# Optimization experiments

Measured on AMD Instinct MI355X. Metric: run time of the kernel, lower is better.

The kernel has to match this reference:

```python
import jax, jax.numpy as jnp
import numpy as np

N = 100000   # nodes
E = 1600000  # edges
IN = 41      # in_channels (21 atom + 20 residue)
ED = 8       # edge_dim
H = 64       # hidden_dim
L = 3        # num_layers
G = 256      # graphs in batch
ATOM = 21
EPS = 1e-5   # GraphNorm eps


def setup_inputs() -> dict:
    key = jax.random.key(0)
    ks = jax.random.split(key, 32)
    s = 0.1
    x = jax.random.normal(ks[0], (N, IN), jnp.float32)
    # make even-index nodes 'ligand' atoms (zero residue part) so both MLP branches fire
    lig = (jnp.arange(N) % 2) == 0
    x = x.at[:, ATOM:].set(jnp.where(lig[:, None], 0.0, x[:, ATOM:]))
    edge_index = jax.random.randint(ks[1], (2, E), 0, N)
    edge_attr = jax.random.normal(ks[2], (E, ED), jnp.float32)
    batch = jnp.sort(jax.random.randint(ks[3], (N,), 0, G))
    p = {
        "lig_W1": s * jax.random.normal(ks[4], (IN, H), jnp.float32),
        "lig_b1": jnp.zeros((H,), jnp.float32),
        "lig_W2": s * jax.random.normal(ks[5], (H, H), jnp.float32),
        "lig_b2": jnp.zeros((H,), jnp.float32),
        "prot_W1": s * jax.random.normal(ks[6], (IN, H), jnp.float32),
        "prot_b1": jnp.zeros((H,), jnp.float32),
        "prot_W2": s * jax.random.normal(ks[7], (H, H), jnp.float32),
        "prot_b2": jnp.zeros((H,), jnp.float32),
        # per-layer stacked params for the 3 GINEConv + GraphNorm blocks
        "conv_We": s * jax.random.normal(ks[8], (L, ED, H), jnp.float32),
        "conv_be": jnp.zeros((L, H), jnp.float32),
        "conv_W1": s * jax.random.normal(ks[9], (L, H, H), jnp.float32),
        "conv_b1": jnp.zeros((L, H), jnp.float32),
        "conv_W2": s * jax.random.normal(ks[10], (L, H, H), jnp.float32),
        "conv_b2": jnp.zeros((L, H), jnp.float32),
        "norm_w": jnp.ones((L, H), jnp.float32),
        "norm_b": jnp.zeros((L, H), jnp.float32),
        "norm_a": jnp.ones((L, H), jnp.float32),  # mean_scale alpha
        "out_W1": s * jax.random.normal(ks[11], (H, H), jnp.float32),
        "out_b1": jnp.zeros((H,), jnp.float32),
        "out_W2": s * jax.random.normal(ks[12], (H, 1), jnp.float32),
        "out_b2": jnp.zeros((1,), jnp.float32),
    }
    return dict(x=x, edge_index=edge_index, edge_attr=edge_attr, batch=batch, **p)


def reference(x, edge_index, edge_attr, batch,
              lig_W1, lig_b1, lig_W2, lig_b2,
              prot_W1, prot_b1, prot_W2, prot_b2,
              conv_We, conv_be, conv_W1, conv_b1, conv_W2, conv_b2,
              norm_w, norm_b, norm_a,
              out_W1, out_b1, out_W2, out_b2):
    # --- input encoder: ligand vs protein branch by residue-part mask ---
    res_mask = jnp.sum(jnp.abs(x[:, ATOM:]), axis=1) > 1e-6
    h_lig = jax.nn.relu(jax.nn.relu(x @ lig_W1 + lig_b1) @ lig_W2 + lig_b2)
    h_prot = jax.nn.relu(jax.nn.relu(x @ prot_W1 + prot_b1) @ prot_W2 + prot_b2)
    h = jnp.where(res_mask[:, None], h_prot, h_lig)  # [N, H]

    src, dst = edge_index[0], edge_index[1]
    counts = jnp.maximum(jax.ops.segment_sum(jnp.ones((N,), h.dtype), batch,
                                             num_segments=G), 1.0)[:, None]  # [G,1]

    for l in range(L):
        # GINEConv (eps=0): nn(h_i + sum_j relu(h_j + lin(e_ij)))
        e = edge_attr @ conv_We[l] + conv_be[l]           # [E, H]
        msg = jax.nn.relu(h[src] + e)                     # [E, H]
        aggr = jax.ops.segment_sum(msg, dst, num_segments=N)
        z = h + aggr
        h = jax.nn.relu(z @ conv_W1[l] + conv_b1[l]) @ conv_W2[l] + conv_b2[l]
        # GraphNorm: (h - alpha*mean_g) / sqrt(var_g + eps) * w + b
        mean = jax.ops.segment_sum(h, batch, num_segments=G) / counts  # [G, H]
        out = h - norm_a[l] * mean[batch]
        var = jax.ops.segment_sum(out * out, batch, num_segments=G) / counts
        h = norm_w[l] * (out / jnp.sqrt(var + EPS)[batch]) + norm_b[l]
        h = jax.nn.relu(h)

    # global_add_pool + readout (dropout = identity at eval)
    g = jax.ops.segment_sum(h, batch, num_segments=G)  # [G, H]
    out = jax.nn.relu(g @ out_W1 + out_b1) @ out_W2 + out_b2  # [G, 1]
    return out.reshape(-1)
```

## Files before the change

### kernel.cpp

```cpp
#include <hip/hip_runtime.h>

#define NN 100000
#define NE 1600000
#define IN_CH 41
#define EDIM 8
#define H 64
#define GNUM 256
#define ATOM 21
#define EPSV 1e-5f
#define EPW 16
#define NTILE (NN / 16)

#define BSH 9
#define NBK 196
#define DPB 512
#define VPT 8
#define EPB (256 * VPT)
#define NBLK_E ((NE + EPB - 1) / EPB)
#define EPB_P1 (1024 * VPT)
#define NBLK_P1 ((NE + EPB_P1 - 1) / EPB_P1)

typedef unsigned short u16;
typedef unsigned int u32;
typedef unsigned long long u64;
typedef __attribute__((ext_vector_type(8))) short short8;
typedef __attribute__((ext_vector_type(4))) float floatx4;

__device__ __forceinline__ u16 f2bf(float f) {
    u32 u = __float_as_uint(f);
    u32 r = (u + 0x7FFFu + ((u >> 16) & 1u)) >> 16;
    return (u16)r;
}
__device__ __forceinline__ float bf2f(u16 u) {
    return __uint_as_float(((u32)u) << 16);
}
__device__ __forceinline__ floatx4 mfma16(short8 a, short8 b, floatx4 c) {
    return __builtin_amdgcn_mfma_f32_16x16x32_bf16(a, b, c, 0, 0, 0);
}
__device__ __forceinline__ short8 pack_bf8(float4 a, float4 b) {
    short8 s;
    s[0] = (short)f2bf(a.x); s[1] = (short)f2bf(a.y);
    s[2] = (short)f2bf(a.z); s[3] = (short)f2bf(a.w);
    s[4] = (short)f2bf(b.x); s[5] = (short)f2bf(b.y);
    s[6] = (short)f2bf(b.z); s[7] = (short)f2bf(b.w);
    return s;
}

__global__ __launch_bounds__(256) void partition_kernel(
    const float* __restrict__ x, int* __restrict__ ctr,
    int* __restrict__ lig_list, int* __restrict__ prot_list)
{
    const int n = blockIdx.x * 256 + threadIdx.x;
    const int lane = threadIdx.x & 63;
    float m = 0.0f;
    if (n < NN) {
        const float* xr = x + (size_t)n * IN_CH + ATOM;
#pragma unroll
        for (int d = 0; d < IN_CH - ATOM; ++d) m += fabsf(xr[d]);
    }
    const bool valid = n < NN;
    const bool prot = valid && (m > 1e-6f);
    const bool lig = valid && !prot;

    const u64 bl = __ballot(lig);
    const u64 bp = __ballot(prot);
    const u64 below_m = (lane == 63) ? (~0ull >> 1) : ((1ull << lane) - 1ull);
    int base_l = 0, base_p = 0;
    if (lane == 0) {
        if (bl) base_l = atomicAdd(&ctr[0], (int)__popcll(bl));
        if (bp) base_p = atomicAdd(&ctr[1], (int)__popcll(bp));
    }
    base_l = __shfl(base_l, 0, 64);
    base_p = __shfl(base_p, 0, 64);
    if (lig)  lig_list [base_l + (int)__popcll(bl & below_m)] = n;
    if (prot) prot_list[base_p + (int)__popcll(bp & below_m)] = n;
}

__global__ __launch_bounds__(256) void xb_kernel(
    const float* __restrict__ x, u16* __restrict__ xb)
{
    const int id = blockIdx.x * 256 + threadIdx.x;
    if (id >= NN * H) return;
    const int n = id >> 6, d = id & 63;
    xb[id] = (d < IN_CH) ? f2bf(x[(size_t)n * IN_CH + d]) : (u16)0;
}

__global__ __launch_bounds__(256) void prep_w_kernel(
    const float* __restrict__ ligW1, const float* __restrict__ ligW2,
    const float* __restrict__ protW1, const float* __restrict__ protW2,
    const float* __restrict__ convW1, const float* __restrict__ convW2,
    u16* __restrict__ wf)
{
    const int id = blockIdx.x * 256 + threadIdx.x;
    if (id >= 10 * 4096) return;
    const int j = id & 7, l = (id >> 3) & 63, t = (id >> 9) & 3;
    const int c = (id >> 11) & 1, mat = id >> 12;
    const int k = c * 32 + ((l >> 4) * 8) + j;
    const int n = t * 16 + (l & 15);
    const float* src; int K = 64;
    if (mat == 0)      { src = ligW1;  K = IN_CH; }
    else if (mat == 1) { src = ligW2; }
    else if (mat == 2) { src = protW1; K = IN_CH; }
    else if (mat == 3) { src = protW2; }
    else {
        const int layer = (mat - 4) >> 1;
        src = (((mat - 4) & 1) ? convW2 : convW1) + (size_t)layer * H * H;
    }
    wf[id] = (k < K) ? f2bf(src[(size_t)k * H + n]) : (u16)0;
}

__global__ __launch_bounds__(256) void enc_mfma_kernel(
    const int* __restrict__ list, const int* __restrict__ countPtr,
    const u16* __restrict__ xb,
    const u16* __restrict__ w1f, const u16* __restrict__ w2f,
    const float* __restrict__ bia1, const float* __restrict__ bia2,
    float* __restrict__ h, u16* __restrict__ h16)
{
    __shared__ __align__(16) u16 hid[4][16 * 72];
    const int wv = threadIdx.x >> 6;
    const int lane = threadIdx.x & 63;
    const int tile = blockIdx.x * 4 + wv;
    const int count = *countPtr;
    if (tile * 16 >= count) return;
    const int quad = lane >> 4;
    const int mi = lane & 15;
    int idx = tile * 16 + mi;
    if (idx >= count) idx = count - 1;
    const int nid = list[idx];

    const short8 a0 = *(const short8*)(xb + (size_t)nid * H + quad * 8);
    const short8 a1 = *(const short8*)(xb + (size_t)nid * H + 32 + quad * 8);

    floatx4 acc[4];
#pragma unroll
    for (int t = 0; t < 4; ++t) acc[t] = (floatx4){0.f, 0.f, 0.f, 0.f};
#pragma unroll
    for (int t = 0; t < 4; ++t) {
        const short8 b0 = *(const short8*)(w1f + ((size_t)(0 * 4 + t) * 64 + lane) * 8);
        const short8 b1 = *(const short8*)(w1f + ((size_t)(1 * 4 + t) * 64 + lane) * 8);
        acc[t] = mfma16(a0, b0, acc[t]);
        acc[t] = mfma16(a1, b1, acc[t]);
    }

    u16* myh = hid[wv];
#pragma unroll
    for (int t = 0; t < 4; ++t) {
        const float bv = bia1[t * 16 + mi];
#pragma unroll
        for (int r = 0; r < 4; ++r) {
            const float v = fmaxf(acc[t][r] + bv, 0.0f);
            myh[(quad * 4 + r) * 72 + t * 16 + mi] = f2bf(v);
        }
    }
    asm volatile("s_waitcnt lgkmcnt(0)" ::: "memory");

    const short8 c0 = *(const short8*)(myh + mi * 72 + quad * 8);
    const short8 c1 = *(const short8*)(myh + mi * 72 + 32 + quad * 8);

    floatx4 acc2[4];
#pragma unroll
    for (int t = 0; t < 4; ++t) acc2[t] = (floatx4){0.f, 0.f, 0.f, 0.f};
#pragma unroll
    for (int t = 0; t < 4; ++t) {
        const short8 b0 = *(const short8*)(w2f + ((size_t)(0 * 4 + t) * 64 + lane) * 8);
        const short8 b1 = *(const short8*)(w2f + ((size_t)(1 * 4 + t) * 64 + lane) * 8);
        acc2[t] = mfma16(c0, b0, acc2[t]);
        acc2[t] = mfma16(c1, b1, acc2[t]);
    }

#pragma unroll
    for (int t = 0; t < 4; ++t) {
        const float bv = bia2[t * 16 + mi];
#pragma unroll
        for (int r = 0; r < 4; ++r) {
            const int row = quad * 4 + r;
            const int nr = __shfl(nid, row, 64);
            if (tile * 16 + row < count) {
                const float v = fmaxf(acc2[t][r] + bv, 0.0f);
                h[(size_t)nr * H + t * 16 + mi] = v;
                h16[(size_t)nr * H + t * 16 + mi] = f2bf(v);
            }
        }
    }
}

__global__ __launch_bounds__(256) void mlp_mfma_kernel(
    const u16* __restrict__ w1f, const u16* __restrict__ w2f,
    const float* __restrict__ bia1, const float* __restrict__ bia2,
    float* __restrict__ h)
{
    __shared__ __align__(16) u16 hid[4][16 * 72];
    const int wv = threadIdx.x >> 6;
    const int lane = threadIdx.x & 63;
    const int tile = blockIdx.x * 4 + wv;
    if (tile >= NTILE) return;
    const int quad = lane >> 4;
    const int mi = lane & 15;
    const int row = tile * 16 + mi;
    const float* zr = h + (size_t)row * H;

    const float4 f0 = *(const float4*)(zr + quad * 8);
    const float4 f1 = *(const float4*)(zr + quad * 8 + 4);
    const float4 f2 = *(const float4*)(zr + 32 + quad * 8);
    const float4 f3 = *(const float4*)(zr + 32 + quad * 8 + 4);
    const short8 a0 = pack_bf8(f0, f1);
    const short8 a1 = pack_bf8(f2, f3);

    floatx4 acc[4];
#pragma unroll
    for (int t = 0; t < 4; ++t) acc[t] = (floatx4){0.f, 0.f, 0.f, 0.f};
#pragma unroll
    for (int t = 0; t < 4; ++t) {
        const short8 b0 = *(const short8*)(w1f + ((size_t)(0 * 4 + t) * 64 + lane) * 8);
        const short8 b1 = *(const short8*)(w1f + ((size_t)(1 * 4 + t) * 64 + lane) * 8);
        acc[t] = mfma16(a0, b0, acc[t]);
        acc[t] = mfma16(a1, b1, acc[t]);
    }

    u16* myh = hid[wv];
#pragma unroll
    for (int t = 0; t < 4; ++t) {
        const float bv = bia1[t * 16 + mi];
#pragma unroll
        for (int r = 0; r < 4; ++r) {
            const float v = fmaxf(acc[t][r] + bv, 0.0f);
            myh[(quad * 4 + r) * 72 + t * 16 + mi] = f2bf(v);
        }
    }
    asm volatile("s_waitcnt lgkmcnt(0)" ::: "memory");

    const short8 c0 = *(const short8*)(myh + mi * 72 + quad * 8);
    const short8 c1 = *(const short8*)(myh + mi * 72 + 32 + quad * 8);

    floatx4 acc2[4];
#pragma unroll
    for (int t = 0; t < 4; ++t) acc2[t] = (floatx4){0.f, 0.f, 0.f, 0.f};
#pragma unroll
    for (int t = 0; t < 4; ++t) {
        const short8 b0 = *(const short8*)(w2f + ((size_t)(0 * 4 + t) * 64 + lane) * 8);
        const short8 b1 = *(const short8*)(w2f + ((size_t)(1 * 4 + t) * 64 + lane) * 8);
        acc2[t] = mfma16(c0, b0, acc2[t]);
        acc2[t] = mfma16(c1, b1, acc2[t]);
    }

#pragma unroll
    for (int t = 0; t < 4; ++t) {
        const float bv = bia2[t * 16 + mi];
#pragma unroll
        for (int r = 0; r < 4; ++r) {
            const int orow = tile * 16 + quad * 4 + r;
            h[(size_t)orow * H + t * 16 + mi] = acc2[t][r] + bv;
        }
    }
}

__global__ void bounds_kernel(const int* __restrict__ batch, int* __restrict__ start)
{
    int g = blockIdx.x * blockDim.x + threadIdx.x;
    if (g > GNUM) return;
    int lo = 0, hi = NN;
    while (lo < hi) {
        int mid = (lo + hi) >> 1;
        if (batch[mid] < g) lo = mid + 1; else hi = mid;
    }
    start[g] = lo;
}

__global__ __launch_bounds__(256) void bhist_kernel(
    const int* __restrict__ ei, int* __restrict__ gbcount)
{
    __shared__ int cnt[NBK];
    const int t = threadIdx.x;
    if (t < NBK) cnt[t] = 0;
    __syncthreads();
    const int base = blockIdx.x * EPB;
#pragma unroll
    for (int v = 0; v < VPT; ++v) {
        const int e = base + v * 256 + t;
        if (e < NE) atomicAdd(&cnt[ei[NE + e] >> BSH], 1);
    }
    __syncthreads();
    if (t < NBK && cnt[t]) atomicAdd(&gbcount[t], cnt[t]);
}

__global__ __launch_bounds__(256) void bscan_kernel(
    const int* __restrict__ gbcount, int* __restrict__ gstart, int* __restrict__ gcur)
{
    __shared__ int s[256];
    const int t = threadIdx.x;
    int v = (t < NBK) ? gbcount[t] : 0;
    s[t] = v;
    __syncthreads();
#pragma unroll
    for (int off = 1; off < 256; off <<= 1) {
        int tmp = (t >= off) ? s[t - off] : 0;
        __syncthreads();
        s[t] += tmp;
        __syncthreads();
    }
    if (t < NBK) { gstart[t] = s[t] - v; gcur[t] = s[t] - v; }
    if (t == 0) gstart[NBK] = NE;
}

__global__ __launch_bounds__(1024) void p1_kernel(
    const int* __restrict__ ei,
    int* __restrict__ gcur,
    int4* __restrict__ tmp_sde)
{
    __shared__ int cnt[NBK];
    __shared__ int cur[NBK];
    const int t = threadIdx.x;
    if (t < NBK) cnt[t] = 0;
    __syncthreads();
    const int base = blockIdx.x * EPB_P1;
    int dstv[VPT];
#pragma unroll
    for (int v = 0; v < VPT; ++v) {
        const int e = base + v * 1024 + t;
        dstv[v] = -1;
        if (e < NE) {
            dstv[v] = ei[NE + e];
            atomicAdd(&cnt[dstv[v] >> BSH], 1);
        }
    }
    __syncthreads();
    if (t < NBK) cur[t] = cnt[t] ? atomicAdd(&gcur[t], cnt[t]) : 0;
    __syncthreads();
#pragma unroll
    for (int v = 0; v < VPT; ++v) {
        const int e = base + v * 1024 + t;
        if (e < NE) {
            const int b = dstv[v] >> BSH;
            const int pos = atomicAdd(&cur[b], 1);
            tmp_sde[pos] = make_int4(ei[e], dstv[v], e, 0);
        }
    }
}

__global__ __launch_bounds__(1024) void sort_kernel(
    const int4* __restrict__ tmp_sde, const float* __restrict__ ea,
    const int* __restrict__ gstart,
    int2* __restrict__ perm2, uint4* __restrict__ eab)
{
    __shared__ int hist[DPB];
    __shared__ int cursor[DPB];
    const int b = blockIdx.x;
    const int t = threadIdx.x;
    const int s = gstart[b], e = gstart[b + 1];
    const int dbase = b << BSH;

    if (t < DPB) hist[t] = 0;
    __syncthreads();
    for (int i = s + t; i < e; i += 1024)
        atomicAdd(&hist[tmp_sde[i].y - dbase], 1);
    __syncthreads();
    if (t < DPB) cursor[t] = hist[t];
    __syncthreads();
#pragma unroll
    for (int off = 1; off < DPB; off <<= 1) {
        int v = (t < DPB && t >= off) ? cursor[t - off] : 0;
        __syncthreads();
        if (t < DPB) cursor[t] += v;
        __syncthreads();
    }
    if (t < DPB) cursor[t] = s + cursor[t] - hist[t];
    __syncthreads();
    for (int i = s + t; i < e; i += 1024) {
        const int4 sde = tmp_sde[i];
        const float4* e4 = (const float4*)(ea + (size_t)sde.z * EDIM);
        const float4 a = e4[0], bb = e4[1];
        uint4 u;
        u.x = (u32)f2bf(a.x) | ((u32)f2bf(a.y) << 16);
        u.y = (u32)f2bf(a.z) | ((u32)f2bf(a.w) << 16);
        u.z = (u32)f2bf(bb.x) | ((u32)f2bf(bb.y) << 16);
        u.w = (u32)f2bf(bb.z) | ((u32)f2bf(bb.w) << 16);
        const int pos = atomicAdd(&cursor[sde.y - dbase], 1);
        perm2[pos] = make_int2(sde.x, sde.y);
        eab[pos] = u;
    }
}

__global__ __launch_bounds__(256) void aggr_kernel(
    const int2* __restrict__ perm2,
    const u32* __restrict__ eab32,
    const float* __restrict__ We, const float* __restrict__ be,
    const u16* __restrict__ h16, float* __restrict__ h)
{
    const int lane = threadIdx.x & 63;
    const int chunk = blockIdx.x * 4 + (threadIdx.x >> 6);
    const int base = chunk * EPW;

    float we_r[EDIM];
#pragma unroll
    for (int d = 0; d < EDIM; ++d) we_r[d] = We[d * H + lane];
    const float be_r = be[lane];

    const int2 pd = perm2[base + (lane & 15)];
    const u32 eu = eab32[(size_t)base * 4 + lane];

    float hv[EPW];
#pragma unroll
    for (int j = 0; j < EPW; ++j) {
        const int sj = __builtin_amdgcn_readlane(pd.x, j);
        hv[j] = bf2f(h16[(size_t)sj * H + lane]);
    }

    float acc = 0.0f;
    int cur = __builtin_amdgcn_readlane(pd.y, 0);
#pragma unroll
    for (int j = 0; j < EPW; ++j) {
        const int dj = __builtin_amdgcn_readlane(pd.y, j);
        float msg = be_r;
#pragma unroll
        for (int p = 0; p < 4; ++p) {
            const u32 w2 = __builtin_amdgcn_readlane(eu, j * 4 + p);
            msg = fmaf(__uint_as_float(w2 << 16), we_r[2 * p], msg);
            msg = fmaf(__uint_as_float(w2 & 0xffff0000u), we_r[2 * p + 1], msg);
        }
        if (dj != cur) {
            unsafeAtomicAdd(&h[(size_t)cur * H + lane], acc);
            acc = 0.0f;
            cur = dj;
        }
        acc += fmaxf(hv[j] + msg, 0.0f);
    }
    unsafeAtomicAdd(&h[(size_t)cur * H + lane], acc);
}

__global__ __launch_bounds__(1024) void graphnorm_kernel(
    float* __restrict__ h, u16* __restrict__ h16,
    const int* __restrict__ start,
    const float* __restrict__ w, const float* __restrict__ b,
    const float* __restrict__ a,
    float* __restrict__ pool, int do_pool)
{
    __shared__ float red1[16][H], red2[16][H];
    __shared__ float amean_s[H], rstd_s[H];
    const int g = blockIdx.x;
    const int lane = threadIdx.x & 63;
    const int wv = threadIdx.x >> 6;
    const int s = start[g], e = start[g + 1];

    float s1 = 0.f, s2 = 0.f;
    for (int i = s + wv; i < e; i += 16) {
        float v = h[(size_t)i * H + lane];
        s1 += v; s2 += v * v;
    }
    red1[wv][lane] = s1; red2[wv][lane] = s2;
    __syncthreads();
    if (threadIdx.x < H) {
        float t1 = 0.f, t2 = 0.f;
#pragma unroll
        for (int k = 0; k < 16; ++k) { t1 += red1[k][lane]; t2 += red2[k][lane]; }
        float cnt = fmaxf((float)(e - s), 1.0f);
        float mean = t1 / cnt;
        float alpha = a[lane];
        float var = t2 / cnt - (2.0f * alpha - alpha * alpha) * mean * mean;
        var = fmaxf(var, 0.0f);
        amean_s[lane] = alpha * mean;
        rstd_s[lane] = rsqrtf(var + EPSV);
    }
    __syncthreads();
    const float am = amean_s[lane], rstd = rstd_s[lane];
    const float ww = w[lane], bb = b[lane];
    float ps = 0.f;
    for (int i = s + wv; i < e; i += 16) {
        float v = (h[(size_t)i * H + lane] - am) * rstd * ww + bb;
        v = fmaxf(v, 0.0f);
        h[(size_t)i * H + lane] = v;
        h16[(size_t)i * H + lane] = f2bf(v);
        ps += v;
    }
    if (do_pool && e > s) unsafeAtomicAdd(&pool[g * H + lane], ps);
}

__global__ __launch_bounds__(64) void final_kernel(
    const float* __restrict__ pool,
    const float* __restrict__ W1, const float* __restrict__ b1,
    const float* __restrict__ W2, const float* __restrict__ b2,
    float* __restrict__ out)
{
    const int g = blockIdx.x;
    const int lane = threadIdx.x;
    const float gv = pool[g * H + lane];
    float acc = b1[lane];
#pragma unroll
    for (int d = 0; d < H; ++d)
        acc = fmaf(__shfl(gv, d, 64), W1[d * H + lane], acc);
    float r = fmaxf(acc, 0.0f);
    float v = r * W2[lane];
#pragma unroll
    for (int o = 32; o > 0; o >>= 1) v += __shfl_xor(v, o, 64);
    if (lane == 0) out[g] = v + b2[0];
}

extern "C" void kernel_launch(void* const* d_in, const int* in_sizes, int n_in,
                              void* d_out, int out_size, void* d_ws, size_t ws_size,
                              hipStream_t stream)
{
    const float* x      = (const float*)d_in[0];
    const int*   ei     = (const int*)  d_in[1];
    const float* ea     = (const float*)d_in[2];
    const int*   batch  = (const int*)  d_in[3];
    const float* ligW1  = (const float*)d_in[4];
    const float* ligb1  = (const float*)d_in[5];
    const float* ligW2  = (const float*)d_in[6];
    const float* ligb2  = (const float*)d_in[7];
    const float* protW1 = (const float*)d_in[8];
    const float* protb1 = (const float*)d_in[9];
    const float* protW2 = (const float*)d_in[10];
    const float* protb2 = (const float*)d_in[11];
    const float* convWe = (const float*)d_in[12];
    const float* convbe = (const float*)d_in[13];
    const float* convW1 = (const float*)d_in[14];
    const float* convb1 = (const float*)d_in[15];
    const float* convW2 = (const float*)d_in[16];
    const float* convb2 = (const float*)d_in[17];
    const float* normw  = (const float*)d_in[18];
    const float* normb  = (const float*)d_in[19];
    const float* norma  = (const float*)d_in[20];
    const float* outW1  = (const float*)d_in[21];
    const float* outb1  = (const float*)d_in[22];
    const float* outW2  = (const float*)d_in[23];
    const float* outb2  = (const float*)d_in[24];

    float* out = (float*)d_out;

    float* h         = (float*)d_ws;
    uint4* eab       = (uint4*)(h + (size_t)NN * H);
    int2*  perm2     = (int2*)(eab + (size_t)NE);
    u16*   h16       = (u16*)(perm2 + (size_t)NE);
    u16*   xb        = h16 + (size_t)NN * H;
    u16*   wf        = xb + (size_t)NN * H;
    int4*  tmp_sde   = (int4*)h;

    int*   ctr       = (int*)(wf + 40960);
    int*   gbcount   = ctr + 2;
    float* pool      = (float*)(gbcount + NBK);
    int*   gstart    = (int*)(pool + GNUM * H);
    int*   gcur      = gstart + (NBK + 1);
    int*   start     = gcur + NBK;
    int*   lig_list  = start + (GNUM + 1);
    int*   prot_list = lig_list + NN;

    hipMemsetAsync(ctr, 0, ((size_t)2 + NBK + GNUM * H) * sizeof(int), stream);

    xb_kernel<<<(NN * H + 255) / 256, 256, 0, stream>>>(x, xb);
    prep_w_kernel<<<(10 * 4096 + 255) / 256, 256, 0, stream>>>(
        ligW1, ligW2, protW1, protW2, convW1, convW2, wf);
    partition_kernel<<<(NN + 255) / 256, 256, 0, stream>>>(x, ctr, lig_list, prot_list);
    bounds_kernel<<<2, 256, 0, stream>>>(batch, start);

    bhist_kernel<<<NBLK_E, 256, 0, stream>>>(ei, gbcount);
    bscan_kernel<<<1, 256, 0, stream>>>(gbcount, gstart, gcur);
    p1_kernel<<<NBLK_P1, 1024, 0, stream>>>(ei, gcur, tmp_sde);
    sort_kernel<<<NBK, 1024, 0, stream>>>(tmp_sde, ea, gstart, perm2, eab);

    const int enc_blocks = (NTILE + 3) / 4;
    enc_mfma_kernel<<<enc_blocks, 256, 0, stream>>>(
        lig_list, &ctr[0], xb, wf + 0 * 4096, wf + 1 * 4096, ligb1, ligb2, h, h16);
    enc_mfma_kernel<<<enc_blocks, 256, 0, stream>>>(
        prot_list, &ctr[1], xb, wf + 2 * 4096, wf + 3 * 4096, protb1, protb2, h, h16);

    const int aggr_blocks = NE / EPW / 4;
    const int mlp_blocks = (NTILE + 3) / 4;
    for (int l = 0; l < 3; ++l) {
        aggr_kernel<<<aggr_blocks, 256, 0, stream>>>(
            perm2, (const u32*)eab,
            convWe + (size_t)l * EDIM * H, convbe + (size_t)l * H, h16, h);
        mlp_mfma_kernel<<<mlp_blocks, 256, 0, stream>>>(
            wf + (size_t)(4 + 2 * l) * 4096, wf + (size_t)(5 + 2 * l) * 4096,
            convb1 + (size_t)l * H, convb2 + (size_t)l * H, h);
        graphnorm_kernel<<<GNUM, 1024, 0, stream>>>(
            h, h16, start, normw + (size_t)l * H, normb + (size_t)l * H,
            norma + (size_t)l * H, pool, (l == 2) ? 1 : 0);
    }
    final_kernel<<<GNUM, 64, 0, stream>>>(pool, outW1, outb1, outW2, outb2, out);
}
```

Measured before the change: 614.6 us.

## Pre-convert edge attrs to bf16 and stage per-quarter sort output in LDS

Edge attributes are converted to packed bf16 in a separate coalesced pass, into scratch space that h16 uses later. The sort kernel then gathers 16-byte records instead of 32-byte fp32 rows. The sort kernel now processes each destination bucket in four 128-node quarters and stages records in shared memory, so perm2 and eab are written contiguously. A direct-write fallback handles quarters that overflow the stage. The cost is four rescans of the bucket's tmp_sde records, more barriers, and an extra kernel launch. xb_kernel is moved after the sort because its buffer region is reused as scratch.

After: 603.7 us. No clear change (-1.8%).

```diff
diff --git a/kernel.cpp b/kernel.cpp
--- a/kernel.cpp
+++ b/kernel.cpp
@@ -13,7 +13,8 @@
 
 #define BSH 9
 #define NBK 196
-#define DPB 512
+#define QD 128
+#define SCAP 2560
 #define VPT 8
 #define EPB (256 * VPT)
 #define NBLK_E ((NE + EPB - 1) / EPB)
@@ -83,6 +84,21 @@
     if (id >= NN * H) return;
     const int n = id >> 6, d = id & 63;
     xb[id] = (d < IN_CH) ? f2bf(x[(size_t)n * IN_CH + d]) : (u16)0;
+}
+
+__global__ __launch_bounds__(256) void ea2b_kernel(
+    const float* __restrict__ ea, uint4* __restrict__ eab16g)
+{
+    const int e = blockIdx.x * 256 + threadIdx.x;
+    if (e >= NE) return;
+    const float4* e4 = (const float4*)(ea + (size_t)e * EDIM);
+    const float4 a = e4[0], b = e4[1];
+    uint4 u;
+    u.x = (u32)f2bf(a.x) | ((u32)f2bf(a.y) << 16);
+    u.y = (u32)f2bf(a.z) | ((u32)f2bf(a.w) << 16);
+    u.z = (u32)f2bf(b.x) | ((u32)f2bf(b.y) << 16);
+    u.w = (u32)f2bf(b.z) | ((u32)f2bf(b.w) << 16);
+    eab16g[e] = u;
 }
 
 __global__ __launch_bounds__(256) void prep_w_kernel(
@@ -338,45 +354,74 @@
 }
 
 __global__ __launch_bounds__(1024) void sort_kernel(
-    const int4* __restrict__ tmp_sde, const float* __restrict__ ea,
+    const int4* __restrict__ tmp_sde, const uint4* __restrict__ eab16g,
     const int* __restrict__ gstart,
     int2* __restrict__ perm2, uint4* __restrict__ eab)
 {
-    __shared__ int hist[DPB];
-    __shared__ int cursor[DPB];
+    __shared__ int hist[QD];
+    __shared__ int cursor[QD];
+    __shared__ int qcnt_s;
+    __shared__ __align__(16) int4 stage[SCAP];
     const int b = blockIdx.x;
     const int t = threadIdx.x;
     const int s = gstart[b], e = gstart[b + 1];
     const int dbase = b << BSH;
 
-    if (t < DPB) hist[t] = 0;
-    __syncthreads();
-    for (int i = s + t; i < e; i += 1024)
-        atomicAdd(&hist[tmp_sde[i].y - dbase], 1);
-    __syncthreads();
-    if (t < DPB) cursor[t] = hist[t];
-    __syncthreads();
-#pragma unroll
-    for (int off = 1; off < DPB; off <<= 1) {
-        int v = (t < DPB && t >= off) ? cursor[t - off] : 0;
+    int qprev = 0;
+    for (int q = 0; q < 4; ++q) {
+        const int qlo = dbase + q * QD;
+        if (t < QD) hist[t] = 0;
         __syncthreads();
-        if (t < DPB) cursor[t] += v;
+        for (int i = s + t; i < e; i += 1024) {
+            const u32 rd = (u32)(tmp_sde[i].y - qlo);
+            if (rd < QD) atomicAdd(&hist[rd], 1);
+        }
         __syncthreads();
-    }
-    if (t < DPB) cursor[t] = s + cursor[t] - hist[t];
-    __syncthreads();
-    for (int i = s + t; i < e; i += 1024) {
-        const int4 sde = tmp_sde[i];
-        const float4* e4 = (const float4*)(ea + (size_t)sde.z * EDIM);
-        const float4 a = e4[0], bb = e4[1];
-        uint4 u;
-        u.x = (u32)f2bf(a.x) | ((u32)f2bf(a.y) << 16);
-        u.y = (u32)f2bf(a.z) | ((u32)f2bf(a.w) << 16);
-        u.z = (u32)f2bf(bb.x) | ((u32)f2bf(bb.y) << 16);
-        u.w = (u32)f2bf(bb.z) | ((u32)f2bf(bb.w) << 16);
-        const int pos = atomicAdd(&cursor[sde.y - dbase], 1);
-        perm2[pos] = make_int2(sde.x, sde.y);
-        eab[pos] = u;
+        if (t < QD) cursor[t] = hist[t];
+        __syncthreads();
+#pragma unroll
+        for (int off = 1; off < QD; off <<= 1) {
+            int v = (t < QD && t >= off) ? cursor[t - off] : 0;
+            __syncthreads();
+            if (t < QD) cursor[t] += v;
+            __syncthreads();
+        }
+        if (t == QD - 1) qcnt_s = cursor[QD - 1];
+        if (t < QD) cursor[t] -= hist[t];
+        __syncthreads();
+        const int qcnt = qcnt_s;
+        const int base = s + qprev;
+
+        if (qcnt <= SCAP) {
+            for (int i = s + t; i < e; i += 1024) {
+                const int4 rec = tmp_sde[i];
+                const u32 rd = (u32)(rec.y - qlo);
+                if (rd < QD) {
+                    const int slot = atomicAdd(&cursor[rd], 1);
+                    stage[slot] = rec;
+                }
+            }
+            __syncthreads();
+            for (int i = t; i < qcnt; i += 1024) {
+                const int4 rec = stage[i];
+                perm2[base + i] = make_int2(rec.x, rec.y);
+                eab[base + i] = eab16g[rec.z];
+            }
+        } else {
+            if (t < QD) cursor[t] += base;
+            __syncthreads();
+            for (int i = s + t; i < e; i += 1024) {
+                const int4 rec = tmp_sde[i];
+                const u32 rd = (u32)(rec.y - qlo);
+                if (rd < QD) {
+                    const int pos = atomicAdd(&cursor[rd], 1);
+                    perm2[pos] = make_int2(rec.x, rec.y);
+                    eab[pos] = eab16g[rec.z];
+                }
+            }
+        }
+        qprev += qcnt;
+        __syncthreads();
     }
 }
 
@@ -533,6 +578,7 @@
     u16*   xb        = h16 + (size_t)NN * H;
     u16*   wf        = xb + (size_t)NN * H;
     int4*  tmp_sde   = (int4*)h;
+    uint4* eab16g    = (uint4*)h16;
 
     int*   ctr       = (int*)(wf + 40960);
     int*   gbcount   = ctr + 2;
@@ -545,7 +591,6 @@
 
     hipMemsetAsync(ctr, 0, ((size_t)2 + NBK + GNUM * H) * sizeof(int), stream);
 
-    xb_kernel<<<(NN * H + 255) / 256, 256, 0, stream>>>(x, xb);
     prep_w_kernel<<<(10 * 4096 + 255) / 256, 256, 0, stream>>>(
         ligW1, ligW2, protW1, protW2, convW1, convW2, wf);
     partition_kernel<<<(NN + 255) / 256, 256, 0, stream>>>(x, ctr, lig_list, prot_list);
@@ -553,9 +598,11 @@
 
     bhist_kernel<<<NBLK_E, 256, 0, stream>>>(ei, gbcount);
     bscan_kernel<<<1, 256, 0, stream>>>(gbcount, gstart, gcur);
+    ea2b_kernel<<<(NE + 255) / 256, 256, 0, stream>>>(ea, eab16g);
     p1_kernel<<<NBLK_P1, 1024, 0, stream>>>(ei, gcur, tmp_sde);
-    sort_kernel<<<NBK, 1024, 0, stream>>>(tmp_sde, ea, gstart, perm2, eab);
-
+    sort_kernel<<<NBK, 1024, 0, stream>>>(tmp_sde, eab16g, gstart, perm2, eab);
+
+    xb_kernel<<<(NN * H + 255) / 256, 256, 0, stream>>>(x, xb);
     const int enc_blocks = (NTILE + 3) / 4;
     enc_mfma_kernel<<<enc_blocks, 256, 0, stream>>>(
         lig_list, &ctr[0], xb, wf + 0 * 4096, wf + 1 * 4096, ligb1, ligb2, h, h16);
```
